# Optimization experiments

Measured on AMD Instinct MI355X. Metric: run time of the kernel, lower is better.

Reference implementation:

```python
import jax, jax.numpy as jnp
import numpy as np

N = 100000
IN_CH = 128
HID = 16
HEADS = 8
OUT_CH = 16
E = 1600000
NEG_SLOPE = 0.2


def glorot(key, shape, fan_in, fan_out):
    lim = jnp.sqrt(6.0 / (fan_in + fan_out)).astype(jnp.float32)
    return jax.random.uniform(key, shape, jnp.float32, -lim, lim)


def setup_inputs() -> dict:
    key = jax.random.key(0)
    ks = jax.random.split(key, 10)
    x = jax.random.normal(ks[0], (N, IN_CH), jnp.float32)
    edge_index = jax.random.randint(ks[1], (2, E), 0, N, jnp.int32)
    # layer 1: GATConv(IN_CH, HID, heads=8), concat=True
    W1 = glorot(ks[2], (IN_CH, HEADS * HID), IN_CH, HEADS * HID)
    att_src1 = glorot(ks[3], (HEADS, HID), HID, 1)
    att_dst1 = glorot(ks[4], (HEADS, HID), HID, 1)
    b1 = jnp.zeros((HEADS * HID,), jnp.float32)
    # layer 2: GATConv(HID*8, OUT_CH, heads=1)
    W2 = glorot(ks[5], (HEADS * HID, OUT_CH), HEADS * HID, OUT_CH)
    att_src2 = glorot(ks[6], (1, OUT_CH), OUT_CH, 1)
    att_dst2 = glorot(ks[7], (1, OUT_CH), OUT_CH, 1)
    b2 = jnp.zeros((OUT_CH,), jnp.float32)
    return {"x": x, "edge_index": edge_index, "W1": W1, "att_src1": att_src1,
            "att_dst1": att_dst1, "b1": b1, "W2": W2, "att_src2": att_src2,
            "att_dst2": att_dst2, "b2": b2}


def gat_layer(x, src, tgt, W, a_src, a_dst, bias, heads, ch, n):
    # h: [N, H, C]
    h = (x @ W).reshape(n, heads, ch)
    alpha_s = jnp.sum(h * a_src[None], axis=-1)  # [N, H]
    alpha_d = jnp.sum(h * a_dst[None], axis=-1)  # [N, H]
    # per-edge attention logit (message flows src -> tgt)
    e = jax.nn.leaky_relu(alpha_s[src] + alpha_d[tgt], NEG_SLOPE)  # [E, H]
    # segment softmax over target node neighborhoods (stable)
    m = jax.ops.segment_max(e, tgt, num_segments=n)  # [N, H]
    e = jnp.exp(e - m[tgt])
    denom = jax.ops.segment_sum(e, tgt, num_segments=n)
    alpha = e / (denom[tgt] + 1e-16)  # [E, H]
    # weighted scatter-add of source features
    out = jax.ops.segment_sum(h[src] * alpha[:, :, None], tgt, num_segments=n)
    return out.reshape(n, heads * ch) + bias


def reference(x, edge_index, W1, att_src1, att_dst1, b1, W2, att_src2, att_dst2, b2):
    n = x.shape[0]
    loops = jnp.arange(n, dtype=edge_index.dtype)
    src = jnp.concatenate([edge_index[0], loops])
    tgt = jnp.concatenate([edge_index[1], loops])
    h = gat_layer(x, src, tgt, W1, att_src1, att_dst1, b1, HEADS, HID, n)
    h = jax.nn.elu(h)
    out = gat_layer(h, src, tgt, W2, att_src2, att_dst2, b2, 1, OUT_CH, n)
    return out
```

## Files before the change

### kernel.cpp

```cpp
#include <hip/hip_runtime.h>
#include <hip/hip_fp16.h>
#include <math.h>

#define IN_CH 128
#define HEADS 8
#define HID 16
#define OUT_CH 16
#define NEG 0.2f
#define NPB 256
#define MAXBUCK 400
#define AST 136

__device__ __forceinline__ float lrelu(float x){ return x > 0.f ? x : NEG * x; }
__device__ __forceinline__ float elu_fast(float x){ return x > 0.f ? x : __expf(x) - 1.f; }

typedef _Float16 half8 __attribute__((ext_vector_type(8)));
typedef float    f32x4 __attribute__((ext_vector_type(4)));

__global__ __launch_bounds__(256) void k_bhist(const int* __restrict__ tgt, int E, int nbuck, int epb,
                                               int* __restrict__ bcnt){
    __shared__ int hist[MAXBUCK];
    int tid = threadIdx.x;
    for (int i = tid; i < nbuck; i += 256) hist[i] = 0;
    __syncthreads();
    int start = blockIdx.x * epb, end = min(start + epb, E);
    for (int e = start + tid; e < end; e += 256) atomicAdd(&hist[tgt[e] >> 8], 1);
    __syncthreads();
    for (int i = tid; i < nbuck; i += 256) if (hist[i]) atomicAdd(&bcnt[i], hist[i]);
}

__global__ void k_bscan(const int* __restrict__ bcnt, int nbuck, int E,
                        int* __restrict__ boffs, int* __restrict__ bcur){
    __shared__ int s[512];
    int t = threadIdx.x;
    int v = (t < nbuck) ? bcnt[t] : 0;
    int orig = v;
    s[t] = v; __syncthreads();
    for (int off = 1; off < 512; off <<= 1){
        int u = (t >= off) ? s[t - off] : 0;
        __syncthreads();
        v += u; s[t] = v; __syncthreads();
    }
    if (t < nbuck){ boffs[t] = v - orig; bcur[t] = v - orig; }
    if (t == 0) boffs[nbuck] = E;
}

__global__ __launch_bounds__(256) void k_bscatter(const int* __restrict__ ei, int E, int nbuck, int epb,
                                                  int* __restrict__ bcur, int2* __restrict__ ebuck){
    __shared__ int hist[MAXBUCK];
    __shared__ int base[MAXBUCK];
    int tid = threadIdx.x;
    for (int i = tid; i < nbuck; i += 256) hist[i] = 0;
    __syncthreads();
    int start = blockIdx.x * epb, end = min(start + epb, E);
    for (int e = start + tid; e < end; e += 256) atomicAdd(&hist[ei[E + e] >> 8], 1);
    __syncthreads();
    for (int i = tid; i < nbuck; i += 256){
        base[i] = hist[i] ? atomicAdd(&bcur[i], hist[i]) : 0;
        hist[i] = 0;
    }
    __syncthreads();
    for (int e = start + tid; e < end; e += 256){
        int s = ei[e], t = ei[E + e];
        int b = t >> 8;
        int r = atomicAdd(&hist[b], 1);
        ebuck[base[b] + r] = make_int2(s, t);
    }
}

__global__ __launch_bounds__(256) void k_csr(const int2* __restrict__ ebuck, const int* __restrict__ boffs,
                                             int N, int E,
                                             int* __restrict__ offs, int* __restrict__ esrc){
    __shared__ int cnt[256];
    __shared__ int sscan[256];
    __shared__ int wcur[256];
    int b = blockIdx.x;
    int tid = threadIdx.x;
    int n0 = b * 256;
    int nn = min(256, N - n0);
    cnt[tid] = (tid < nn) ? 1 : 0;
    __syncthreads();
    int e0 = boffs[b], e1 = boffs[b + 1];
    for (int e = e0 + tid; e < e1; e += 256) atomicAdd(&cnt[ebuck[e].y & 255], 1);
    __syncthreads();
    int v = cnt[tid], orig = v;
    sscan[tid] = v; __syncthreads();
    for (int off = 1; off < 256; off <<= 1){
        int u = (tid >= off) ? sscan[tid - off] : 0;
        __syncthreads();
        v += u; sscan[tid] = v; __syncthreads();
    }
    int excl = v - orig;
    int gbase = e0 + n0;
    if (tid < nn){
        offs[n0 + tid] = gbase + excl;
        esrc[gbase + excl] = n0 + tid;
    }
    wcur[tid] = excl + 1;
    __syncthreads();
    for (int e = e0 + tid; e < e1; e += 256){
        int2 p = ebuck[e];
        int r = atomicAdd(&wcur[p.y & 255], 1);
        esrc[gbase + r] = p.x;
    }
    if (b == 0 && tid == 0) offs[N] = E + N;
}

__global__ __launch_bounds__(256) void k_gemm1(const float* __restrict__ x, const float* __restrict__ W1,
                                               __half* __restrict__ h1, int N){
    __shared__ _Float16 sA[64*AST];
    __shared__ _Float16 sB[128*AST];
    int tid = threadIdx.x;
    for (int i = tid; i < 128*32; i += 256){
        int k = i >> 5, c0 = (i & 31) * 4;
        float4 w4 = *(const float4*)(W1 + k*128 + c0);
        sB[(c0+0)*AST + k] = (_Float16)w4.x;
        sB[(c0+1)*AST + k] = (_Float16)w4.y;
        sB[(c0+2)*AST + k] = (_Float16)w4.z;
        sB[(c0+3)*AST + k] = (_Float16)w4.w;
    }
    int row0 = blockIdx.x * 64;
    #pragma unroll
    for (int i = 0; i < 8; ++i){
        int q = i*256 + tid;
        int r = q >> 5, seg = q & 31;
        float4 v = make_float4(0.f,0.f,0.f,0.f);
        if (row0 + r < N) v = *(const float4*)(x + (size_t)(row0+r)*128 + seg*4);
        _Float16* dst = &sA[r*AST + seg*4];
        dst[0]=(_Float16)v.x; dst[1]=(_Float16)v.y; dst[2]=(_Float16)v.z; dst[3]=(_Float16)v.w;
    }
    __syncthreads();
    int wave = tid >> 6, lane = tid & 63;
    int m = lane & 15, quad = lane >> 4;
    int rbase = wave * 16;
    f32x4 acc[8] = {};
    #pragma unroll
    for (int kc = 0; kc < 4; ++kc){
        int kb = kc*32 + quad*8;
        half8 a = *(half8*)(&sA[(rbase + m)*AST + kb]);
        #pragma unroll
        for (int t = 0; t < 8; ++t){
            half8 b = *(half8*)(&sB[(t*16 + m)*AST + kb]);
            acc[t] = __builtin_amdgcn_mfma_f32_16x16x32_f16(a, b, acc[t], 0, 0, 0);
        }
    }
    #pragma unroll
    for (int t = 0; t < 8; ++t){
        #pragma unroll
        for (int j = 0; j < 4; ++j){
            int r = row0 + rbase + quad*4 + j;
            if (r < N) h1[(size_t)r*128 + t*16 + m] = __float2half(acc[t][j]);
        }
    }
}

struct H8 { __half2 v[8]; };

__global__ void k_alpha1(const __half2* __restrict__ h1h, const float* __restrict__ asrc, const float* __restrict__ adst,
                         float2* __restrict__ asw, float* __restrict__ ad1,
                         unsigned char* __restrict__ h1q, int N){
    int idx = blockIdx.x*blockDim.x + threadIdx.x;
    if (idx >= N*HEADS) return;
    int h = idx & 7;
    int n = idx >> 3;
    H8 blk = *(const H8*)(h1h + (size_t)n*64 + h*8);
    const float2* sp = (const float2*)(asrc + h*16);
    const float2* dp = (const float2*)(adst + h*16);
    float fv[16];
    float ss = 0.f, dd = 0.f;
    #pragma unroll
    for (int j = 0; j < 8; ++j){
        float2 v = __half22float2(blk.v[j]);
        fv[2*j] = v.x; fv[2*j+1] = v.y;
        float2 a = sp[j], b = dp[j];
        ss += v.x*a.x + v.y*a.y;
        dd += v.x*b.x + v.y*b.y;
    }
    float mx = 1e-12f;
    #pragma unroll
    for (int k = 0; k < 16; ++k) mx = fmaxf(mx, fabsf(fv[k]));
    float rs = 127.f / mx;
    unsigned int w[4];
    #pragma unroll
    for (int d = 0; d < 4; ++d){
        unsigned int b0 = (unsigned int)((int)rintf(fv[4*d+0]*rs) + 128);
        unsigned int b1 = (unsigned int)((int)rintf(fv[4*d+1]*rs) + 128);
        unsigned int b2 = (unsigned int)((int)rintf(fv[4*d+2]*rs) + 128);
        unsigned int b3 = (unsigned int)((int)rintf(fv[4*d+3]*rs) + 128);
        w[d] = b0 | (b1 << 8) | (b2 << 16) | (b3 << 24);
    }
    asw[idx] = make_float2(ss, mx * (1.f/127.f));
    ad1[idx] = dd;
    *(uint4*)(h1q + (size_t)idx*16) = make_uint4(w[0], w[1], w[2], w[3]);
}

__global__ __launch_bounds__(256) void k_agg1(const unsigned char* __restrict__ h1q, const float2* __restrict__ asw,
                                              const float* __restrict__ ad1,
                                              const int* __restrict__ offs, const int* __restrict__ esrc,
                                              const float* __restrict__ b1, __half2* __restrict__ hl2h,
                                              int nbase, int nend){
    int wv = threadIdx.x >> 6;
    int l  = threadIdx.x & 63;
    int nsub = l >> 5;
    int slot = (l >> 3) & 3;
    int c    = l & 7;
    int n = nbase + blockIdx.x*8 + wv*2 + nsub;
    bool alive = (n < nend);
    float adc = 0.f;
    int e0 = 0, deg = 0;
    if (alive){
        adc = ad1[n*8 + c];
        e0 = offs[n];
        deg = offs[n+1] - e0;
    }
    int degmax = max(deg, __shfl_xor(deg, 32));

    float acc[16] = {};
    float den = 0.f;
    float dq  = 0.f;
    for (int i = 0; i < degmax; i += 8){
        int j0 = i + slot, j1 = i + 4 + slot;
        bool v0 = j0 < deg, v1 = j1 < deg;
        int iA = e0 + (v0 ? j0 : 0);
        int iB = e0 + (v1 ? j1 : 0);
        int s0 = esrc[iA], s1 = esrc[iB];
        float2 aw0 = asw[s0*8 + c];
        float2 aw1 = asw[s1*8 + c];
        uint4 q0 = *(const uint4*)(h1q + (size_t)s0*128 + c*16);
        uint4 q1 = *(const uint4*)(h1q + (size_t)s1*128 + c*16);
        float w0 = v0 ? __expf(lrelu(aw0.x + adc)) : 0.f;
        float w1 = v1 ? __expf(lrelu(aw1.x + adc)) : 0.f;
        float wq0 = w0 * aw0.y;
        float wq1 = w1 * aw1.y;
        den += w0 + w1;
        dq  += wq0 + wq1;
        const unsigned int* u0 = (const unsigned int*)&q0;
        const unsigned int* u1 = (const unsigned int*)&q1;
        #pragma unroll
        for (int d = 0; d < 4; ++d){
            unsigned int a = u0[d], b = u1[d];
            acc[4*d+0] += wq0 * (float)(a & 255u);
            acc[4*d+1] += wq0 * (float)((a >> 8) & 255u);
            acc[4*d+2] += wq0 * (float)((a >> 16) & 255u);
            acc[4*d+3] += wq0 * (float)(a >> 24);
            acc[4*d+0] += wq1 * (float)(b & 255u);
            acc[4*d+1] += wq1 * (float)((b >> 8) & 255u);
            acc[4*d+2] += wq1 * (float)((b >> 16) & 255u);
            acc[4*d+3] += wq1 * (float)(b >> 24);
        }
    }
    den += __shfl_xor(den, 8);  den += __shfl_xor(den, 16);
    dq  += __shfl_xor(dq, 8);   dq  += __shfl_xor(dq, 16);
    #pragma unroll
    for (int k = 0; k < 16; ++k){
        acc[k] += __shfl_xor(acc[k], 8);
        acc[k] += __shfl_xor(acc[k], 16);
    }
    if (!alive) return;
    float rd = 1.f / (den + 1e-16f);
    float bias128 = 128.f * dq;
    float sel0, sel1, sel2, sel3;
    {
        float a0 = (slot & 1) ? acc[4]  : acc[0];
        float b0 = (slot & 1) ? acc[12] : acc[8];
        sel0 = (slot & 2) ? b0 : a0;
        float a1 = (slot & 1) ? acc[5]  : acc[1];
        float b1v = (slot & 1) ? acc[13] : acc[9];
        sel1 = (slot & 2) ? b1v : a1;
        float a2 = (slot & 1) ? acc[6]  : acc[2];
        float b2v = (slot & 1) ? acc[14] : acc[10];
        sel2 = (slot & 2) ? b2v : a2;
        float a3 = (slot & 1) ? acc[7]  : acc[3];
        float b3v = (slot & 1) ? acc[15] : acc[11];
        sel3 = (slot & 2) ? b3v : a3;
    }
    float4 b4 = *(const float4*)(b1 + c*16 + slot*4);
    float v0 = elu_fast((sel0 - bias128)*rd + b4.x);
    float v1 = elu_fast((sel1 - bias128)*rd + b4.y);
    float v2 = elu_fast((sel2 - bias128)*rd + b4.z);
    float v3 = elu_fast((sel3 - bias128)*rd + b4.w);
    __half2 q0h = __floats2half2_rn(v0, v1);
    __half2 q1h = __floats2half2_rn(v2, v3);
    float2 ov;
    *(__half2*)&ov.x = q0h; *(__half2*)&ov.y = q1h;
    *(float2*)(hl2h + (size_t)n*64 + c*8 + slot*2) = ov;
}

#define FMA4(acc, a, b) { acc.x += (a)*(b).x; acc.y += (a)*(b).y; acc.z += (a)*(b).z; acc.w += (a)*(b).w; }

__global__ __launch_bounds__(256) void k_gemm2(const __half2* __restrict__ hl2h, const float* __restrict__ W2,
                                               const float* __restrict__ asrc2, const float* __restrict__ adst2,
                                               __half2* __restrict__ h2h, float* __restrict__ as2, float* __restrict__ ad2,
                                               int N){
    __shared__ float sX[64*132];
    __shared__ float sW2[128*16];
    int tid = threadIdx.x;
    for (int i = tid; i < 128*16; i += 256) sW2[i] = W2[i];
    int row0 = blockIdx.x * 64;
    #pragma unroll
    for (int i = 0; i < 4; ++i){
        int q = i*256 + tid;
        int r = q >> 4, seg = q & 15;
        float4 raw = make_float4(0.f,0.f,0.f,0.f);
        if (row0 + r < N) raw = ((const float4*)(hl2h + (size_t)(row0+r)*64))[seg];
        const __half2* hp = (const __half2*)&raw;
        float* dst = &sX[r*132 + seg*8];
        #pragma unroll
        for (int j = 0; j < 4; ++j){
            float2 f = __half22float2(hp[j]);
            dst[2*j] = f.x; dst[2*j+1] = f.y;
        }
    }
    __syncthreads();
    int nd = tid >> 2;
    int cq = tid & 3, c0 = cq*4;
    int n = row0 + nd;
    float4 acc = make_float4(0.f,0.f,0.f,0.f);
    #pragma unroll 4
    for (int k4 = 0; k4 < 32; ++k4){
        float4 a  = *(const float4*)(&sX[nd*132 + k4*4]);
        float4 w0 = *(const float4*)(&sW2[(k4*4+0)*16 + c0]);
        float4 w1 = *(const float4*)(&sW2[(k4*4+1)*16 + c0]);
        float4 w2 = *(const float4*)(&sW2[(k4*4+2)*16 + c0]);
        float4 w3 = *(const float4*)(&sW2[(k4*4+3)*16 + c0]);
        FMA4(acc, a.x, w0); FMA4(acc, a.y, w1); FMA4(acc, a.z, w2); FMA4(acc, a.w, w3);
    }
    float ps = acc.x*asrc2[c0] + acc.y*asrc2[c0+1] + acc.z*asrc2[c0+2] + acc.w*asrc2[c0+3];
    float pd = acc.x*adst2[c0] + acc.y*adst2[c0+1] + acc.z*adst2[c0+2] + acc.w*adst2[c0+3];
    ps += __shfl_xor(ps, 1); ps += __shfl_xor(ps, 2);
    pd += __shfl_xor(pd, 1); pd += __shfl_xor(pd, 2);
    if (n < N){
        __half2 p0 = __floats2half2_rn(acc.x, acc.y);
        __half2 p1 = __floats2half2_rn(acc.z, acc.w);
        float2 ov;
        *(__half2*)&ov.x = p0; *(__half2*)&ov.y = p1;
        *(float2*)(h2h + (size_t)n*8 + cq*2) = ov;
        if (cq == 0){ as2[n] = ps; ad2[n] = pd; }
    }
}

__global__ __launch_bounds__(256) void k_agg2(const __half2* __restrict__ h2h, const float* __restrict__ as2v,
                                              const float* __restrict__ ad2v,
                                              const int* __restrict__ offs, const int* __restrict__ esrc,
                                              const float* __restrict__ b2, float* __restrict__ out, int N){
    int n = blockIdx.x*4 + (threadIdx.x >> 6);
    if (n >= N) return;
    int l = threadIdx.x & 63;
    int e0 = offs[n], e1 = offs[n+1];
    float ad = ad2v[n];
    int eo = l >> 3, c2 = l & 7;
    float ax = 0.f, ay = 0.f, den = 0.f;
    for (int e = e0 + eo; e < e1; e += 8){
        int s = esrc[e];
        float w = __expf(lrelu(as2v[s] + ad));
        den += w;
        float2 f = __half22float2(h2h[(size_t)s*8 + c2]);
        ax += w * f.x; ay += w * f.y;
    }
    ax += __shfl_xor(ax, 8);  ay += __shfl_xor(ay, 8);  den += __shfl_xor(den, 8);
    ax += __shfl_xor(ax, 16); ay += __shfl_xor(ay, 16); den += __shfl_xor(den, 16);
    ax += __shfl_xor(ax, 32); ay += __shfl_xor(ay, 32); den += __shfl_xor(den, 32);
    if (eo == 0){
        float rd = 1.f / (den + 1e-16f);
        float2 bb = *(const float2*)(b2 + c2*2);
        float2 o = make_float2(ax*rd + bb.x, ay*rd + bb.y);
        *(float2*)(out + (size_t)n*16 + c2*2) = o;
    }
}

extern "C" void kernel_launch(void* const* d_in, const int* in_sizes, int n_in,
                              void* d_out, int out_size, void* d_ws, size_t ws_size,
                              hipStream_t stream){
    const float* x     = (const float*)d_in[0];
    const int*   ei    = (const int*)  d_in[1];
    const float* W1    = (const float*)d_in[2];
    const float* asrc1 = (const float*)d_in[3];
    const float* adst1 = (const float*)d_in[4];
    const float* b1    = (const float*)d_in[5];
    const float* W2    = (const float*)d_in[6];
    const float* asrc2 = (const float*)d_in[7];
    const float* adst2 = (const float*)d_in[8];
    const float* b2    = (const float*)d_in[9];
    float* out = (float*)d_out;

    const int N = in_sizes[0] / IN_CH;
    const int E = in_sizes[1] / 2;
    const int ETOT = E + N;
    const int NBUCK = (N + NPB - 1) / NPB;

    char* p = (char*)d_ws;
    auto alloc = [&](size_t bytes) -> char* {
        char* r = p; p += (bytes + 255) & ~(size_t)255; return r;
    };
    __half2* h1h  = (__half2*)alloc((size_t)N * 64 * 4);
    __half2* hl2h = (__half2*)alloc((size_t)N * 64 * 4);
    unsigned char* h1q = (unsigned char*)alloc((size_t)N * 128);
    float2* asw  = (float2*)alloc((size_t)N * 8 * 8);
    float* ad1   = (float*)alloc((size_t)N * 8 * 4);
    __half2* h2h = (__half2*)alloc((size_t)N * 8 * 4);
    float* as2   = (float*)alloc((size_t)N * 4);
    float* ad2   = (float*)alloc((size_t)N * 4);
    int*   bcnt  = (int*)  alloc((size_t)MAXBUCK * 4);
    int*   boffs = (int*)  alloc((size_t)(MAXBUCK + 1) * 4);
    int*   bcur  = (int*)  alloc((size_t)MAXBUCK * 4);
    int*   offs  = (int*)  alloc((size_t)(N + 1) * 4);
    int*   esrc  = (int*)  alloc((size_t)ETOT * 4);
    int2*  ebuck = (int2*)hl2h;

    (void)hipMemsetAsync(bcnt, 0, (size_t)NBUCK * 4, stream);

    const int GPART = 512;
    const int epb = (E + GPART - 1) / GPART;

    k_bhist   <<<GPART, 256, 0, stream>>>(ei + E, E, NBUCK, epb, bcnt);
    k_bscan   <<<1,     512, 0, stream>>>(bcnt, NBUCK, E, boffs, bcur);
    k_bscatter<<<GPART, 256, 0, stream>>>(ei, E, NBUCK, epb, bcur, ebuck);
    k_csr     <<<NBUCK, 256, 0, stream>>>(ebuck, boffs, N, E, offs, esrc);

    k_gemm1  <<<(N + 63) / 64, 256, 0, stream>>>(x, W1, (__half*)h1h, N);
    k_alpha1 <<<(N * HEADS + 255) / 256, 256, 0, stream>>>(h1h, asrc1, adst1, asw, ad1, h1q, N);

    const int NH = ((N / 2) + 7) & ~7;
    k_agg1 <<<(NH + 7) / 8, 256, 0, stream>>>(h1q, asw, ad1, offs, esrc, b1, hl2h, 0, NH);
    k_agg1 <<<((N - NH) + 7) / 8, 256, 0, stream>>>(h1q, asw, ad1, offs, esrc, b1, hl2h, NH, N);

    k_gemm2  <<<(N + 63) / 64, 256, 0, stream>>>(hl2h, W2, asrc2, adst2, h2h, as2, ad2, N);
    k_agg2   <<<(N + 3) / 4, 256, 0, stream>>>(h2h, as2, ad2, offs, esrc, b2, out, N);
}
```

Before: 330.4 us.

## Make gemm1 persistent with double-buffered LDS and register prefetch of x tiles

New measurement: 308.3 us. 6.7% less time.

```diff
diff --git a/kernel.cpp b/kernel.cpp
--- a/kernel.cpp
+++ b/kernel.cpp
@@ -107,50 +107,69 @@
 }
 
 __global__ __launch_bounds__(256) void k_gemm1(const float* __restrict__ x, const float* __restrict__ W1,
-                                               __half* __restrict__ h1, int N){
-    __shared__ _Float16 sA[64*AST];
+                                               __half* __restrict__ h1, int N, int NT){
     __shared__ _Float16 sB[128*AST];
+    __shared__ _Float16 sA[2][64*AST];
     int tid = threadIdx.x;
-    for (int i = tid; i < 128*32; i += 256){
-        int k = i >> 5, c0 = (i & 31) * 4;
-        float4 w4 = *(const float4*)(W1 + k*128 + c0);
-        sB[(c0+0)*AST + k] = (_Float16)w4.x;
-        sB[(c0+1)*AST + k] = (_Float16)w4.y;
-        sB[(c0+2)*AST + k] = (_Float16)w4.z;
-        sB[(c0+3)*AST + k] = (_Float16)w4.w;
-    }
-    int row0 = blockIdx.x * 64;
+    for (int i = tid; i < 128*128; i += 256){
+        int k = i >> 7, c = i & 127;
+        sB[c*AST + k] = (_Float16)W1[i];
+    }
+    int wave = tid >> 6, lane = tid & 63;
+    int m = lane & 15, quad = lane >> 4;
+    int rbase = wave * 16;
+
+    float4 vr[8];
+    int tile = blockIdx.x;
     #pragma unroll
     for (int i = 0; i < 8; ++i){
         int q = i*256 + tid;
         int r = q >> 5, seg = q & 31;
-        float4 v = make_float4(0.f,0.f,0.f,0.f);
-        if (row0 + r < N) v = *(const float4*)(x + (size_t)(row0+r)*128 + seg*4);
-        _Float16* dst = &sA[r*AST + seg*4];
-        dst[0]=(_Float16)v.x; dst[1]=(_Float16)v.y; dst[2]=(_Float16)v.z; dst[3]=(_Float16)v.w;
-    }
-    __syncthreads();
-    int wave = tid >> 6, lane = tid & 63;
-    int m = lane & 15, quad = lane >> 4;
-    int rbase = wave * 16;
-    f32x4 acc[8] = {};
-    #pragma unroll
-    for (int kc = 0; kc < 4; ++kc){
-        int kb = kc*32 + quad*8;
-        half8 a = *(half8*)(&sA[(rbase + m)*AST + kb]);
+        int row = tile*64 + r;
+        vr[i] = make_float4(0.f,0.f,0.f,0.f);
+        if (tile < NT && row < N) vr[i] = *(const float4*)(x + (size_t)row*128 + seg*4);
+    }
+    int b = 0;
+    for (; tile < NT; tile += gridDim.x){
+        #pragma unroll
+        for (int i = 0; i < 8; ++i){
+            int q = i*256 + tid;
+            int r = q >> 5, seg = q & 31;
+            _Float16* dst = &sA[b][r*AST + seg*4];
+            dst[0]=(_Float16)vr[i].x; dst[1]=(_Float16)vr[i].y;
+            dst[2]=(_Float16)vr[i].z; dst[3]=(_Float16)vr[i].w;
+        }
+        __syncthreads();
+        int tn = tile + gridDim.x;
+        #pragma unroll
+        for (int i = 0; i < 8; ++i){
+            int q = i*256 + tid;
+            int r = q >> 5, seg = q & 31;
+            int row = tn*64 + r;
+            vr[i] = make_float4(0.f,0.f,0.f,0.f);
+            if (tn < NT && row < N) vr[i] = *(const float4*)(x + (size_t)row*128 + seg*4);
+        }
+        f32x4 acc[8] = {};
+        #pragma unroll
+        for (int kc = 0; kc < 4; ++kc){
+            int kb = kc*32 + quad*8;
+            half8 a = *(half8*)(&sA[b][(rbase + m)*AST + kb]);
+            #pragma unroll
+            for (int t = 0; t < 8; ++t){
+                half8 bb = *(half8*)(&sB[(t*16 + m)*AST + kb]);
+                acc[t] = __builtin_amdgcn_mfma_f32_16x16x32_f16(a, bb, acc[t], 0, 0, 0);
+            }
+        }
+        int row0 = tile*64;
         #pragma unroll
         for (int t = 0; t < 8; ++t){
-            half8 b = *(half8*)(&sB[(t*16 + m)*AST + kb]);
-            acc[t] = __builtin_amdgcn_mfma_f32_16x16x32_f16(a, b, acc[t], 0, 0, 0);
-        }
-    }
-    #pragma unroll
-    for (int t = 0; t < 8; ++t){
-        #pragma unroll
-        for (int j = 0; j < 4; ++j){
-            int r = row0 + rbase + quad*4 + j;
-            if (r < N) h1[(size_t)r*128 + t*16 + m] = __float2half(acc[t][j]);
-        }
+            #pragma unroll
+            for (int j = 0; j < 4; ++j){
+                int r = row0 + rbase + quad*4 + j;
+                if (r < N) h1[(size_t)r*128 + t*16 + m] = __float2half(acc[t][j]);
+            }
+        }
+        b ^= 1;
     }
 }
 
@@ -417,7 +436,9 @@
     k_bscatter<<<GPART, 256, 0, stream>>>(ei, E, NBUCK, epb, bcur, ebuck);
     k_csr     <<<NBUCK, 256, 0, stream>>>(ebuck, boffs, N, E, offs, esrc);
 
-    k_gemm1  <<<(N + 63) / 64, 256, 0, stream>>>(x, W1, (__half*)h1h, N);
+    const int NT = (N + 63) / 64;
+    const int G1 = NT < 512 ? NT : 512;
+    k_gemm1  <<<G1, 256, 0, stream>>>(x, W1, (__half*)h1h, N, NT);
     k_alpha1 <<<(N * HEADS + 255) / 256, 256, 0, stream>>>(h1h, asrc1, adst1, asw, ad1, h1q, N);
 
     const int NH = ((N / 2) + 7) & ~7;
```
